# Kernel optimization log

Hardware: AMD Instinct MI355X
Metric: run time of the kernel (lower is better)

## Reference

```python
import jax, jax.numpy as jnp
import numpy as np

E = 1024   # embed_dim
H = 16     # num_heads
R = 256    # rank
HD = E // H
B, S = 2, 2048


def setup_inputs() -> dict:
    key = jax.random.key(0)
    ks = jax.random.split(key, 20)
    sc = 0.02
    d = {
        'query': jax.random.normal(ks[0], (B, S, E), jnp.float32),
        'key':   jax.random.normal(ks[1], (B, S, E), jnp.float32),
        'value': jax.random.normal(ks[2], (B, S, E), jnp.float32),
    }
    names = ['q', 'k', 'v', 'o']
    i = 3
    for n in names:
        d[f'W{n}_lo'] = jax.random.normal(ks[i], (E, R), jnp.float32) * sc; i += 1
        d[f'b{n}_lo'] = jnp.zeros((R,), jnp.float32)
        d[f'W{n}_hi'] = jax.random.normal(ks[i], (R, E), jnp.float32) * sc; i += 1
        d[f'b{n}_hi'] = jnp.zeros((E,), jnp.float32)
    return d


def _lowrank(x, W_lo, b_lo, W_hi, b_hi):
    # Linear(E->R) then Linear(R->E)
    return (x @ W_lo + b_lo) @ W_hi + b_hi


def reference(query, key, value,
              Wq_lo, bq_lo, Wq_hi, bq_hi,
              Wk_lo, bk_lo, Wk_hi, bk_hi,
              Wv_lo, bv_lo, Wv_hi, bv_hi,
              Wo_lo, bo_lo, Wo_hi, bo_hi):
    b, s, _ = query.shape
    q = _lowrank(query, Wq_lo, bq_lo, Wq_hi, bq_hi)
    k = _lowrank(key,   Wk_lo, bk_lo, Wk_hi, bk_hi)
    v = _lowrank(value, Wv_lo, bv_lo, Wv_hi, bv_hi)
    # (B, S, E) -> (B, H, S, HD)
    q = q.reshape(b, s, H, HD).transpose(0, 2, 1, 3)
    k = k.reshape(b, s, H, HD).transpose(0, 2, 1, 3)
    v = v.reshape(b, s, H, HD).transpose(0, 2, 1, 3)
    scores = jnp.einsum('bhqd,bhkd->bhqk', q, k) / jnp.sqrt(jnp.float32(HD))
    attn = jax.nn.softmax(scores, axis=-1)  # dropout p=0.0 -> identity
    out = jnp.einsum('bhqk,bhkd->bhqd', attn, v)
    out = out.transpose(0, 2, 1, 3).reshape(b, s, E)
    return _lowrank(out, Wo_lo, bo_lo, Wo_hi, bo_hi)
```

## Files before the change

### kernel.cpp

```cpp
#include <hip/hip_runtime.h>

namespace {

constexpr int kE  = 1024;
constexpr int kH  = 16;
constexpr int kR  = 256;
constexpr int kHD = 64;
constexpr int kB  = 2;
constexpr int kS  = 2048;
constexpr int kM  = kB * kS;

typedef float  floatx4 __attribute__((ext_vector_type(4)));
typedef short  short8  __attribute__((ext_vector_type(8)));
typedef short  short4  __attribute__((ext_vector_type(4)));
typedef unsigned int uint2v __attribute__((ext_vector_type(2)));

__device__ inline short f2bf(float f) {
  union { float f; unsigned u; } x{f};
  unsigned r = x.u + 0x7FFF + ((x.u >> 16) & 1);
  return (short)(r >> 16);
}

__device__ inline unsigned cvt_pk_bf16(float a, float b) {
#if defined(__HIP_DEVICE_COMPILE__)
  unsigned r;
  asm("v_cvt_pk_bf16_f32 %0, %1, %2" : "=v"(r) : "v"(a), "v"(b));
  return r;
#else
  return (unsigned)(unsigned short)f2bf(a) | ((unsigned)(unsigned short)f2bf(b) << 16);
#endif
}

__device__ inline short4 pack2(unsigned a, unsigned b) {
  union { uint2v u; short4 s; } x;
  x.u[0] = a; x.u[1] = b;
  return x.s;
}

__device__ inline short8 pack4(unsigned a, unsigned b, unsigned c, unsigned d) {
  union { unsigned u[4]; short8 s; } x;
  x.u[0] = a; x.u[1] = b; x.u[2] = c; x.u[3] = d;
  return x.s;
}

__device__ inline float fexp2(float x) {
#if defined(__HIP_DEVICE_COMPILE__) && __has_builtin(__builtin_amdgcn_exp2f)
  return __builtin_amdgcn_exp2f(x);
#else
  return exp2f(x);
#endif
}

__device__ inline void async_copy16(const void* g, void* l) {
  __builtin_amdgcn_global_load_lds(
      (const __attribute__((address_space(1))) unsigned int*)g,
      (__attribute__((address_space(3))) unsigned int*)l,
      16, 0, 0);
}

__device__ inline int xcd_swz256(int bid) {
  return ((bid & 7) << 5) | (bid >> 3);
}

#if defined(__HIP_DEVICE_COMPILE__)
  #if __has_builtin(__builtin_amdgcn_mfma_f32_16x16x16bf16_1k)
    #define MFMA16(a, b, c) __builtin_amdgcn_mfma_f32_16x16x16bf16_1k(a, b, c, 0, 0, 0)
  #elif __has_builtin(__builtin_amdgcn_mfma_f32_16x16x16_bf16)
    #define MFMA16(a, b, c) __builtin_amdgcn_mfma_f32_16x16x16_bf16(a, b, c, 0, 0, 0)
  #else
    #error "no 16x16x16 bf16 MFMA builtin on device"
  #endif
#else
  #define MFMA16(a, b, c) (c)
#endif

struct PrepArgs { const float* src[8]; short* dst[8]; };

__global__ __launch_bounds__(256) void prep_weights(PrepArgs pa) {
  const int id = blockIdx.y;
  const bool lo = (id & 1) == 0;
  const int K = lo ? 1024 : 256;
  const int N = lo ? 256 : 1024;
  const int tiles_k = K >> 6;
  const int k0 = (blockIdx.x % tiles_k) * 64;
  const int n0 = (blockIdx.x / tiles_k) * 64;
  const float* src = pa.src[id];
  short* dst = pa.dst[id];

  __shared__ float tile[64][68];
  const int t  = threadIdx.x;
  const int c4 = (t & 15) * 4;
  const int r  = t >> 4;

#pragma unroll
  for (int i = 0; i < 4; ++i) {
    const int rk = r + i * 16;
    *(float4*)&tile[rk][c4] = *(const float4*)&src[(size_t)(k0 + rk) * N + n0 + c4];
  }
  __syncthreads();
#pragma unroll
  for (int i = 0; i < 4; ++i) {
    const int rn = r + i * 16;
    short4 o = { f2bf(tile[c4 + 0][rn]), f2bf(tile[c4 + 1][rn]),
                 f2bf(tile[c4 + 2][rn]), f2bf(tile[c4 + 3][rn]) };
    *(short4*)&dst[(size_t)(n0 + rn) * K + k0 + c4] = o;
  }
}

struct GemmArgs {
  const short* A[3]; const short* Bt[3]; const float* bias[3];
  void* C[3]; float scale[3];
};

template <int N, int K, int BM, int BN, int MODE>
__global__ __launch_bounds__(256) void gemm_bf16(GemmArgs args) {
  constexpr int TILES_N = N / BN;
  constexpr int WTM = BM / 2, WTN = BN / 2;
  constexpr int FI = WTM / 16, FJ = WTN / 16;
  constexpr int AROUNDS = (BM * 64) / 4096;
  constexpr int BROUNDS = (BN * 64) / 4096;
  static_assert((kM / BM) * (N / BN) == 256, "swizzle assumes nwg=256");

  const int z = blockIdx.y;
  const int swz = xcd_swz256(blockIdx.x);
  const int row0 = (swz / TILES_N) * BM;
  const int col0 = (swz % TILES_N) * BN;
  const short* A  = args.A[z];
  const short* Bt = args.Bt[z];
  const float* bias = args.bias[z];
  const float scale = args.scale[z];

  __shared__ short As[BM * 32];
  __shared__ short Bs[BN * 32];

  const int t    = threadIdx.x;
  const int wave = t >> 6;
  const int lane = t & 63;
  const int lq   = lane & 15;
  const int quad = lane >> 4;
  const int wm0  = (wave >> 1) * WTM;
  const int wn0  = (wave & 1) * WTN;

  const int srow = t >> 2;
  const int scol = (t & 3) * 8;

  floatx4 acc[FI][FJ] = {};

  for (int kk = 0; kk < K; kk += 32) {
#pragma unroll
    for (int r = 0; r < AROUNDS; ++r)
      async_copy16(A + (size_t)(row0 + r * 64 + srow) * K + kk + scol,
                   (char*)As + r * 4096 + wave * 1024);
#pragma unroll
    for (int r = 0; r < BROUNDS; ++r)
      async_copy16(Bt + (size_t)(col0 + r * 64 + srow) * K + kk + scol,
                   (char*)Bs + r * 4096 + wave * 1024);
    __syncthreads();

    short8 af[FI], bf[FJ];
#pragma unroll
    for (int i = 0; i < FI; ++i)
      af[i] = *(const short8*)((const char*)As + ((wm0 + i * 16 + lq) * 64 + quad * 16));
#pragma unroll
    for (int j = 0; j < FJ; ++j)
      bf[j] = *(const short8*)((const char*)Bs + ((wn0 + j * 16 + lq) * 64 + quad * 16));
#pragma unroll
    for (int i = 0; i < FI; ++i)
#pragma unroll
      for (int j = 0; j < FJ; ++j)
        acc[i][j] = __builtin_amdgcn_mfma_f32_16x16x32_bf16(af[i], bf[j], acc[i][j], 0, 0, 0);
    __syncthreads();
  }

#pragma unroll
  for (int i = 0; i < FI; ++i) {
    const int rbase = row0 + wm0 + i * 16 + quad * 4;
#pragma unroll
    for (int j = 0; j < FJ; ++j) {
      const int col = col0 + wn0 + j * 16 + lq;
      const float bj = bias[col];
      if (MODE == 2) {
        float* C = (float*)args.C[z];
#pragma unroll
        for (int r = 0; r < 4; ++r)
          C[(size_t)(rbase + r) * N + col] = (acc[i][j][r] + bj) * scale;
      } else if (MODE == 1) {
        short* C = (short*)args.C[z];
        const int h = col >> 6, d = col & 63;
        const int b = rbase >> 11, s = rbase & 2047;
        if (z == 2) {
          short4 o = { f2bf(acc[i][j][0] + bj), f2bf(acc[i][j][1] + bj),
                       f2bf(acc[i][j][2] + bj), f2bf(acc[i][j][3] + bj) };
          *(short4*)&C[((size_t)((b * 16 + h) * 64 + d)) * 2048 + s] = o;
        } else {
#pragma unroll
          for (int r = 0; r < 4; ++r)
            C[((size_t)((b * 16 + h) * 2048 + s + r)) * 64 + d] =
                f2bf((acc[i][j][r] + bj) * scale);
        }
      } else {
        short* C = (short*)args.C[z];
#pragma unroll
        for (int r = 0; r < 4; ++r)
          C[(size_t)(rbase + r) * N + col] = f2bf((acc[i][j][r] + bj) * scale);
      }
    }
  }
}

struct GemmLoArgs {
  const float* A[3]; const short* Bt[3]; const float* bias[3]; short* C[3];
};

__global__ __launch_bounds__(256) void gemm_lo_f32a(GemmLoArgs args) {
  constexpr int N = kR, K = kE, BM = 64, BN = 64;
  constexpr int TILES_N = N / BN;
  constexpr int WTM = BM / 2, WTN = BN / 2;
  constexpr int FI = WTM / 16, FJ = WTN / 16;
  static_assert((kM / BM) * (N / BN) == 256, "swizzle assumes nwg=256");

  const int z = blockIdx.y;
  const int swz = xcd_swz256(blockIdx.x);
  const int row0 = (swz / TILES_N) * BM;
  const int col0 = (swz % TILES_N) * BN;
  const float* A  = args.A[z];
  const short* Bt = args.Bt[z];
  const float* bias = args.bias[z];
  short* C = args.C[z];

  __shared__ float As32[64][36];
  __shared__ short Bs[BN * 32];

  const int t    = threadIdx.x;
  const int wave = t >> 6;
  const int lane = t & 63;
  const int lq   = lane & 15;
  const int quad = lane >> 4;
  const int wm0  = (wave >> 1) * WTM;
  const int wn0  = (wave & 1) * WTN;

  const int arow  = t >> 2;
  const int acolf = (t & 3) * 8;
  const int srow = t >> 2;
  const int scol = (t & 3) * 8;

  floatx4 acc[FI][FJ] = {};

  const float* arow_p = A + (size_t)(row0 + arow) * K + acolf;
  float4 ga0 = *(const float4*)(arow_p);
  float4 ga1 = *(const float4*)(arow_p + 4);

  for (int kk = 0; kk < K; kk += 32) {
    __syncthreads();
    *(float4*)&As32[arow][acolf]     = ga0;
    *(float4*)&As32[arow][acolf + 4] = ga1;
    async_copy16(Bt + (size_t)(col0 + srow) * K + kk + scol,
                 (char*)Bs + wave * 1024);
    __syncthreads();

    if (kk + 32 < K) {
      ga0 = *(const float4*)(arow_p + kk + 32);
      ga1 = *(const float4*)(arow_p + kk + 36);
    }

    short8 af[FI], bf[FJ];
#pragma unroll
    for (int i = 0; i < FI; ++i) {
      const int r = wm0 + i * 16 + lq;
      float4 f0 = *(const float4*)&As32[r][quad * 8];
      float4 f1 = *(const float4*)&As32[r][quad * 8 + 4];
      af[i] = pack4(cvt_pk_bf16(f0.x, f0.y), cvt_pk_bf16(f0.z, f0.w),
                    cvt_pk_bf16(f1.x, f1.y), cvt_pk_bf16(f1.z, f1.w));
    }
#pragma unroll
    for (int j = 0; j < FJ; ++j)
      bf[j] = *(const short8*)((const char*)Bs + ((wn0 + j * 16 + lq) * 64 + quad * 16));
#pragma unroll
    for (int i = 0; i < FI; ++i)
#pragma unroll
      for (int j = 0; j < FJ; ++j)
        acc[i][j] = __builtin_amdgcn_mfma_f32_16x16x32_bf16(af[i], bf[j], acc[i][j], 0, 0, 0);
  }

#pragma unroll
  for (int i = 0; i < FI; ++i) {
    const int rbase = row0 + wm0 + i * 16 + quad * 4;
#pragma unroll
    for (int j = 0; j < FJ; ++j) {
      const int col = col0 + wn0 + j * 16 + lq;
      const float bj = bias[col];
#pragma unroll
      for (int r = 0; r < 4; ++r)
        C[(size_t)(rbase + r) * N + col] = f2bf(acc[i][j][r] + bj);
    }
  }
}

__global__ __launch_bounds__(256) void attn_mfma(
    const short* __restrict__ Qp, const short* __restrict__ Kp,
    const short* __restrict__ Vtp, short* __restrict__ O)
{
  __shared__ short Ks[64][72];
  __shared__ short Vs[64][72];

  const int t    = threadIdx.x;
  const int wave = t >> 6;
  const int lane = t & 63;
  const int lq   = lane & 15;
  const int quad = lane >> 4;

  const int q0 = blockIdx.x * 128;
  const int bh = blockIdx.y;
  const int b  = bh >> 4;
  const int h  = bh & 15;

  short8 qf0[2], qf1[2];
#pragma unroll
  for (int qt = 0; qt < 2; ++qt) {
    const short* qrow = Qp + ((size_t)bh * kS + q0 + wave * 32 + qt * 16 + lq) * 64;
    qf0[qt] = *(const short8*)(qrow + quad * 8);
    qf1[qt] = *(const short8*)(qrow + 32 + quad * 8);
  }

  const short* Kbase = Kp  + (size_t)bh * kS * 64;
  const short* Vbase = Vtp + (size_t)bh * 64 * kS;

  const int srow = wave * 16 + (lane >> 3);
  const int scol = (lane & 7) * 8;

  floatx4 Oacc[4][2] = {};
  float m[2] = {-1e30f, -1e30f};
  float l[2] = {0.f, 0.f};

  short8 gk0 = *(const short8*)(Kbase + (size_t)(srow) * 64 + scol);
  short8 gk1 = *(const short8*)(Kbase + (size_t)(srow + 8) * 64 + scol);
  short8 gv0 = *(const short8*)(Vbase + (size_t)srow * kS + scol);
  short8 gv1 = *(const short8*)(Vbase + (size_t)(srow + 8) * kS + scol);

  for (int kc = 0; kc < kS; kc += 64) {
    __syncthreads();
    *(short8*)&Ks[srow][scol]     = gk0;
    *(short8*)&Ks[srow + 8][scol] = gk1;
    *(short8*)&Vs[srow][scol]     = gv0;
    *(short8*)&Vs[srow + 8][scol] = gv1;
    __syncthreads();

    if (kc + 64 < kS) {
      gk0 = *(const short8*)(Kbase + (size_t)(kc + 64 + srow) * 64 + scol);
      gk1 = *(const short8*)(Kbase + (size_t)(kc + 64 + srow + 8) * 64 + scol);
      gv0 = *(const short8*)(Vbase + (size_t)srow * kS + kc + 64 + scol);
      gv1 = *(const short8*)(Vbase + (size_t)(srow + 8) * kS + kc + 64 + scol);
    }

    floatx4 Sc[4][2];
#pragma unroll
    for (int tt = 0; tt < 4; ++tt) {
      short8 a0 = *(const short8*)&Ks[tt * 16 + lq][quad * 8];
      short8 a1 = *(const short8*)&Ks[tt * 16 + lq][32 + quad * 8];
#pragma unroll
      for (int qt = 0; qt < 2; ++qt) {
        floatx4 c = {};
        c = __builtin_amdgcn_mfma_f32_16x16x32_bf16(a0, qf0[qt], c, 0, 0, 0);
        c = __builtin_amdgcn_mfma_f32_16x16x32_bf16(a1, qf1[qt], c, 0, 0, 0);
        Sc[tt][qt] = c;
      }
    }

    short4 pf[4][2];
#pragma unroll
    for (int qt = 0; qt < 2; ++qt) {
      float x0 = fmaxf(fmaxf(Sc[0][qt][0], Sc[0][qt][1]), fmaxf(Sc[0][qt][2], Sc[0][qt][3]));
      float x1 = fmaxf(fmaxf(Sc[1][qt][0], Sc[1][qt][1]), fmaxf(Sc[1][qt][2], Sc[1][qt][3]));
      float x2 = fmaxf(fmaxf(Sc[2][qt][0], Sc[2][qt][1]), fmaxf(Sc[2][qt][2], Sc[2][qt][3]));
      float x3 = fmaxf(fmaxf(Sc[3][qt][0], Sc[3][qt][1]), fmaxf(Sc[3][qt][2], Sc[3][qt][3]));
      float plane = fmaxf(fmaxf(x0, x1), fmaxf(x2, x3));

      if (!__all(plane <= m[qt] + 10.f)) {
        float mc = fmaxf(plane, __shfl_xor(plane, 16, 64));
        mc = fmaxf(mc, __shfl_xor(mc, 32, 64));
        const float mn = fmaxf(m[qt], mc);
        const float a = fexp2(m[qt] - mn);
        m[qt] = mn;
        l[qt] *= a;
#pragma unroll
        for (int dt = 0; dt < 4; ++dt) Oacc[dt][qt] *= a;
      }

      float ls = 0.f;
#pragma unroll
      for (int tt = 0; tt < 4; ++tt) {
        float p0 = fexp2(Sc[tt][qt][0] - m[qt]);
        float p1 = fexp2(Sc[tt][qt][1] - m[qt]);
        float p2 = fexp2(Sc[tt][qt][2] - m[qt]);
        float p3 = fexp2(Sc[tt][qt][3] - m[qt]);
        ls += (p0 + p1) + (p2 + p3);
        pf[tt][qt] = pack2(cvt_pk_bf16(p0, p1), cvt_pk_bf16(p2, p3));
      }
      l[qt] += ls;
    }

#pragma unroll
    for (int dt = 0; dt < 4; ++dt) {
#pragma unroll
      for (int tt = 0; tt < 4; ++tt) {
        short4 vf = *(const short4*)&Vs[dt * 16 + lq][tt * 16 + quad * 4];
#pragma unroll
        for (int qt = 0; qt < 2; ++qt)
          Oacc[dt][qt] = MFMA16(vf, pf[tt][qt], Oacc[dt][qt]);
      }
    }
  }

#pragma unroll
  for (int qt = 0; qt < 2; ++qt) {
    float lv = l[qt];
    lv += __shfl_xor(lv, 16, 64);
    lv += __shfl_xor(lv, 32, 64);
    const float inv = 1.f / lv;

    short* orow = O + ((size_t)(b * kS + q0 + wave * 32 + qt * 16 + lq)) * kE + h * kHD;
#pragma unroll
    for (int dt = 0; dt < 4; ++dt) {
      short4 o = pack2(cvt_pk_bf16(Oacc[dt][qt][0] * inv, Oacc[dt][qt][1] * inv),
                       cvt_pk_bf16(Oacc[dt][qt][2] * inv, Oacc[dt][qt][3] * inv));
      *(short4*)&orow[dt * 16 + quad * 4] = o;
    }
  }
}

}

extern "C" void kernel_launch(void* const* d_in, const int* in_sizes, int n_in,
                              void* d_out, int out_size, void* d_ws, size_t ws_size,
                              hipStream_t stream) {
  short* ws = (short*)d_ws;
  short* Xq  = ws;
  short* Xk  = Xq  + (size_t)kM * kE;
  short* Xv  = Xk  + (size_t)kM * kE;
  short* Tq  = Xv  + (size_t)kM * kE;
  short* Tk  = Tq  + (size_t)kM * kR;
  short* Tv  = Tk  + (size_t)kM * kR;
  short* Qh  = Tv  + (size_t)kM * kR;
  short* Kh  = Qh  + (size_t)kM * kE;
  short* Vth = Kh  + (size_t)kM * kE;
  short* Ab  = Vth + (size_t)kM * kE;
  short* To  = Ab  + (size_t)kM * kE;
  short* Wt  = To  + (size_t)kM * kR;
  (void)Xk; (void)Xv;

  short* WtArr[8];
  for (int i = 0; i < 8; ++i) WtArr[i] = Wt + (size_t)i * (kE * kR);

  PrepArgs pa;
  const int widx[8] = {3, 5, 7, 9, 11, 13, 15, 17};
  for (int i = 0; i < 8; ++i) { pa.src[i] = (const float*)d_in[widx[i]]; pa.dst[i] = WtArr[i]; }
  prep_weights<<<dim3(64, 8), dim3(256), 0, stream>>>(pa);

  {
    GemmLoArgs ga;
    ga.A[0] = (const float*)d_in[0]; ga.A[1] = (const float*)d_in[1]; ga.A[2] = (const float*)d_in[2];
    ga.Bt[0] = WtArr[0]; ga.Bt[1] = WtArr[2]; ga.Bt[2] = WtArr[4];
    ga.bias[0] = (const float*)d_in[4]; ga.bias[1] = (const float*)d_in[8]; ga.bias[2] = (const float*)d_in[12];
    ga.C[0] = Tq; ga.C[1] = Tk; ga.C[2] = Tv;
    gemm_lo_f32a<<<dim3((kM / 64) * (kR / 64), 3), dim3(256), 0, stream>>>(ga);
  }

  {
    GemmArgs ga;
    ga.A[0] = Tq; ga.A[1] = Tk; ga.A[2] = Tv;
    ga.Bt[0] = WtArr[1]; ga.Bt[1] = WtArr[3]; ga.Bt[2] = WtArr[5];
    ga.bias[0] = (const float*)d_in[6]; ga.bias[1] = (const float*)d_in[10]; ga.bias[2] = (const float*)d_in[14];
    ga.C[0] = Qh; ga.C[1] = Kh; ga.C[2] = Vth;
    ga.scale[0] = 0.125f * 1.44269504088896340736f;
    ga.scale[1] = 1.f; ga.scale[2] = 1.f;
    gemm_bf16<kE, kR, 128, 128, 1><<<dim3((kM / 128) * (kE / 128), 3), dim3(256), 0, stream>>>(ga);
  }

  attn_mfma<<<dim3(kS / 128, kB * kH), dim3(256), 0, stream>>>(Qh, Kh, Vth, Ab);

  {
    GemmArgs ga;
    ga.A[0] = Ab; ga.Bt[0] = WtArr[6];
    ga.bias[0] = (const float*)d_in[16];
    ga.C[0] = To; ga.scale[0] = 1.f;
    gemm_bf16<kR, kE, 64, 64, 0><<<dim3((kM / 64) * (kR / 64), 1), dim3(256), 0, stream>>>(ga);
  }
  {
    GemmArgs ga;
    ga.A[0] = To; ga.Bt[0] = WtArr[7];
    ga.bias[0] = (const float*)d_in[18];
    ga.C[0] = d_out; ga.scale[0] = 1.f;
    gemm_bf16<kE, kR, 128, 128, 2><<<dim3((kM / 128) * (kE / 128), 1), dim3(256), 0, stream>>>(ga);
  }
}
```

Before: 253.5 us.

## Replace LDS-direct async loads with register-prefetched padded LDS tiles in GEMMs

The GEMM kernels stop using global_load_lds async copies. They now prefetch the next K-slice into registers while the current slice is computed, then store it into LDS tiles padded to an 80-byte row pitch to avoid bank conflicts. The trailing barrier per iteration is removed, leaving one barrier pair placed before the stores. This trades extra VGPRs and explicit LDS writes for overlap of global loads with MFMA work and conflict-free fragment reads. Unused workspace pointers and a template parameter are also cleaned up.

```diff
diff --git a/kernel.cpp b/kernel.cpp
--- a/kernel.cpp
+++ b/kernel.cpp
@@ -49,13 +49,6 @@
 #else
   return exp2f(x);
 #endif
-}
-
-__device__ inline void async_copy16(const void* g, void* l) {
-  __builtin_amdgcn_global_load_lds(
-      (const __attribute__((address_space(1))) unsigned int*)g,
-      (__attribute__((address_space(3))) unsigned int*)l,
-      16, 0, 0);
 }
 
 __device__ inline int xcd_swz256(int bid) {
@@ -112,14 +105,16 @@
   void* C[3]; float scale[3];
 };
 
-template <int N, int K, int BM, int BN, int MODE>
+template <int M, int N, int K, int BM, int BN, int MODE>
 __global__ __launch_bounds__(256) void gemm_bf16(GemmArgs args) {
   constexpr int TILES_N = N / BN;
   constexpr int WTM = BM / 2, WTN = BN / 2;
   constexpr int FI = WTM / 16, FJ = WTN / 16;
   constexpr int AROUNDS = (BM * 64) / 4096;
   constexpr int BROUNDS = (BN * 64) / 4096;
-  static_assert((kM / BM) * (N / BN) == 256, "swizzle assumes nwg=256");
+  constexpr int P = 80;
+  static_assert((M / BM) * (N / BN) == 256, "swizzle assumes nwg=256");
+  static_assert(MODE != 1 || M == kM, "MODE1 decode assumes M=4096");
 
   const int z = blockIdx.y;
   const int swz = xcd_swz256(blockIdx.x);
@@ -130,8 +125,8 @@
   const float* bias = args.bias[z];
   const float scale = args.scale[z];
 
-  __shared__ short As[BM * 32];
-  __shared__ short Bs[BN * 32];
+  __shared__ short As[BM * 40];
+  __shared__ short Bs[BN * 40];
 
   const int t    = threadIdx.x;
   const int wave = t >> 6;
@@ -143,33 +138,49 @@
 
   const int srow = t >> 2;
   const int scol = (t & 3) * 8;
+  const int sbyte = (t & 3) * 16;
 
   floatx4 acc[FI][FJ] = {};
 
+  short8 ra[AROUNDS], rb[BROUNDS];
+#pragma unroll
+  for (int r = 0; r < AROUNDS; ++r)
+    ra[r] = *(const short8*)(A + (size_t)(row0 + r * 64 + srow) * K + scol);
+#pragma unroll
+  for (int r = 0; r < BROUNDS; ++r)
+    rb[r] = *(const short8*)(Bt + (size_t)(col0 + r * 64 + srow) * K + scol);
+
   for (int kk = 0; kk < K; kk += 32) {
+    __syncthreads();
 #pragma unroll
     for (int r = 0; r < AROUNDS; ++r)
-      async_copy16(A + (size_t)(row0 + r * 64 + srow) * K + kk + scol,
-                   (char*)As + r * 4096 + wave * 1024);
+      *(short8*)((char*)As + (r * 64 + srow) * P + sbyte) = ra[r];
 #pragma unroll
     for (int r = 0; r < BROUNDS; ++r)
-      async_copy16(Bt + (size_t)(col0 + r * 64 + srow) * K + kk + scol,
-                   (char*)Bs + r * 4096 + wave * 1024);
+      *(short8*)((char*)Bs + (r * 64 + srow) * P + sbyte) = rb[r];
     __syncthreads();
 
+    if (kk + 32 < K) {
+#pragma unroll
+      for (int r = 0; r < AROUNDS; ++r)
+        ra[r] = *(const short8*)(A + (size_t)(row0 + r * 64 + srow) * K + kk + 32 + scol);
+#pragma unroll
+      for (int r = 0; r < BROUNDS; ++r)
+        rb[r] = *(const short8*)(Bt + (size_t)(col0 + r * 64 + srow) * K + kk + 32 + scol);
+    }
+
     short8 af[FI], bf[FJ];
 #pragma unroll
     for (int i = 0; i < FI; ++i)
-      af[i] = *(const short8*)((const char*)As + ((wm0 + i * 16 + lq) * 64 + quad * 16));
+      af[i] = *(const short8*)((const char*)As + ((wm0 + i * 16 + lq) * P + quad * 16));
 #pragma unroll
     for (int j = 0; j < FJ; ++j)
-      bf[j] = *(const short8*)((const char*)Bs + ((wn0 + j * 16 + lq) * 64 + quad * 16));
+      bf[j] = *(const short8*)((const char*)Bs + ((wn0 + j * 16 + lq) * P + quad * 16));
 #pragma unroll
     for (int i = 0; i < FI; ++i)
 #pragma unroll
       for (int j = 0; j < FJ; ++j)
         acc[i][j] = __builtin_amdgcn_mfma_f32_16x16x32_bf16(af[i], bf[j], acc[i][j], 0, 0, 0);
-    __syncthreads();
   }
 
 #pragma unroll
@@ -217,6 +228,7 @@
   constexpr int TILES_N = N / BN;
   constexpr int WTM = BM / 2, WTN = BN / 2;
   constexpr int FI = WTM / 16, FJ = WTN / 16;
+  constexpr int P = 80;
   static_assert((kM / BM) * (N / BN) == 256, "swizzle assumes nwg=256");
 
   const int z = blockIdx.y;
@@ -229,7 +241,7 @@
   short* C = args.C[z];
 
   __shared__ float As32[64][36];
-  __shared__ short Bs[BN * 32];
+  __shared__ short Bs[BN * 40];
 
   const int t    = threadIdx.x;
   const int wave = t >> 6;
@@ -241,26 +253,28 @@
 
   const int arow  = t >> 2;
   const int acolf = (t & 3) * 8;
-  const int srow = t >> 2;
-  const int scol = (t & 3) * 8;
+  const int srow  = t >> 2;
+  const int scol  = (t & 3) * 8;
+  const int sbyte = (t & 3) * 16;
 
   floatx4 acc[FI][FJ] = {};
 
   const float* arow_p = A + (size_t)(row0 + arow) * K + acolf;
   float4 ga0 = *(const float4*)(arow_p);
   float4 ga1 = *(const float4*)(arow_p + 4);
+  short8 rb  = *(const short8*)(Bt + (size_t)(col0 + srow) * K + scol);
 
   for (int kk = 0; kk < K; kk += 32) {
     __syncthreads();
     *(float4*)&As32[arow][acolf]     = ga0;
     *(float4*)&As32[arow][acolf + 4] = ga1;
-    async_copy16(Bt + (size_t)(col0 + srow) * K + kk + scol,
-                 (char*)Bs + wave * 1024);
+    *(short8*)((char*)Bs + srow * P + sbyte) = rb;
     __syncthreads();
 
     if (kk + 32 < K) {
       ga0 = *(const float4*)(arow_p + kk + 32);
       ga1 = *(const float4*)(arow_p + kk + 36);
+      rb  = *(const short8*)(Bt + (size_t)(col0 + srow) * K + kk + 32 + scol);
     }
 
     short8 af[FI], bf[FJ];
@@ -274,7 +288,7 @@
     }
 #pragma unroll
     for (int j = 0; j < FJ; ++j)
-      bf[j] = *(const short8*)((const char*)Bs + ((wn0 + j * 16 + lq) * 64 + quad * 16));
+      bf[j] = *(const short8*)((const char*)Bs + ((wn0 + j * 16 + lq) * P + quad * 16));
 #pragma unroll
     for (int i = 0; i < FI; ++i)
 #pragma unroll
@@ -434,10 +448,7 @@
                               void* d_out, int out_size, void* d_ws, size_t ws_size,
                               hipStream_t stream) {
   short* ws = (short*)d_ws;
-  short* Xq  = ws;
-  short* Xk  = Xq  + (size_t)kM * kE;
-  short* Xv  = Xk  + (size_t)kM * kE;
-  short* Tq  = Xv  + (size_t)kM * kE;
+  short* Tq  = ws;
   short* Tk  = Tq  + (size_t)kM * kR;
   short* Tv  = Tk  + (size_t)kM * kR;
   short* Qh  = Tv  + (size_t)kM * kR;
@@ -446,7 +457,6 @@
   short* Ab  = Vth + (size_t)kM * kE;
   short* To  = Ab  + (size_t)kM * kE;
   short* Wt  = To  + (size_t)kM * kR;
-  (void)Xk; (void)Xv;
 
   short* WtArr[8];
   for (int i = 0; i < 8; ++i) WtArr[i] = Wt + (size_t)i * (kE * kR);
@@ -462,7 +472,7 @@
     ga.Bt[0] = WtArr[0]; ga.Bt[1] = WtArr[2]; ga.Bt[2] = WtArr[4];
     ga.bias[0] = (const float*)d_in[4]; ga.bias[1] = (const float*)d_in[8]; ga.bias[2] = (const float*)d_in[12];
     ga.C[0] = Tq; ga.C[1] = Tk; ga.C[2] = Tv;
-    gemm_lo_f32a<<<dim3((kM / 64) * (kR / 64), 3), dim3(256), 0, stream>>>(ga);
+    gemm_lo_f32a<<<dim3(256, 3), dim3(256), 0, stream>>>(ga);
   }
 
   {
@@ -473,7 +483,7 @@
     ga.C[0] = Qh; ga.C[1] = Kh; ga.C[2] = Vth;
     ga.scale[0] = 0.125f * 1.44269504088896340736f;
     ga.scale[1] = 1.f; ga.scale[2] = 1.f;
-    gemm_bf16<kE, kR, 128, 128, 1><<<dim3((kM / 128) * (kE / 128), 3), dim3(256), 0, stream>>>(ga);
+    gemm_bf16<kM, kE, kR, 128, 128, 1><<<dim3(256, 3), dim3(256), 0, stream>>>(ga);
   }
 
   attn_mfma<<<dim3(kS / 128, kB * kH), dim3(256), 0, stream>>>(Qh, Kh, Vth, Ab);
@@ -483,13 +493,13 @@
     ga.A[0] = Ab; ga.Bt[0] = WtArr[6];
     ga.bias[0] = (const float*)d_in[16];
     ga.C[0] = To; ga.scale[0] = 1.f;
-    gemm_bf16<kR, kE, 64, 64, 0><<<dim3((kM / 64) * (kR / 64), 1), dim3(256), 0, stream>>>(ga);
+    gemm_bf16<kM, kR, kE, 64, 64, 0><<<dim3(256, 1), dim3(256), 0, stream>>>(ga);
   }
   {
     GemmArgs ga;
     ga.A[0] = To; ga.Bt[0] = WtArr[7];
     ga.bias[0] = (const float*)d_in[18];
     ga.C[0] = d_out; ga.scale[0] = 1.f;
-    gemm_bf16<kE, kR, 128, 128, 2><<<dim3((kM / 128) * (kE / 128), 1), dim3(256), 0, stream>>>(ga);
-  }
-}
+    gemm_bf16<kM, kE, kR, 128, 128, 2><<<dim3(256, 1), dim3(256), 0, stream>>>(ga);
+  }
+}
```

After: 243.8 us. 3.8% less time.
